# Optimization experiments

Measured on AMD Instinct MI355X. Metric: run time of the kernel, lower is better.

## Reference

```python
import jax, jax.numpy as jnp
import numpy as np

B, Cin, Cout, H, W, K = 8, 256, 256, 64, 64, 3  # kernel 3x3, stride 1, pad 1, dilation 1
EPS = 1e-5


def setup_inputs() -> dict:
    key = jax.random.key(0)
    k0, k1, k2 = jax.random.split(key, 3)
    x = jax.random.normal(k0, (B, Cin, H, W), jnp.float32)
    # offset-predicting conv (mmcv zero-inits it; use small random weights so offsets are nontrivial)
    w_off = jax.random.normal(k1, (2 * K * K, Cin, K, K), jnp.float32) * 0.01
    b_off = jnp.zeros((2 * K * K,), jnp.float32)
    # main deformable conv weight
    w = jax.random.normal(k2, (Cout, Cin, K, K), jnp.float32) * (1.0 / np.sqrt(Cin * K * K))
    b = jnp.zeros((Cout,), jnp.float32)
    gamma = jnp.ones((Cout,), jnp.float32)
    beta = jnp.zeros((Cout,), jnp.float32)
    return {"x": x, "w_off": w_off, "b_off": b_off, "w": w, "b": b, "gamma": gamma, "beta": beta}


def _deform_fusion(x, w_off, b_off, w, b, gamma, beta):
    Bn, C, Hh, Ww = x.shape
    # 1) predict offsets: [B, 2*K*K, H, W]; channel layout is (dy, dx) per kernel tap
    offset = jax.lax.conv_general_dilated(x, w_off, (1, 1), ((1, 1), (1, 1)))
    offset = offset + b_off[None, :, None, None]
    off = offset.reshape(Bn, K * K, 2, Hh, Ww)
    dy, dx = off[:, :, 0], off[:, :, 1]  # each [B, K*K, H, W]

    # 2) sampling positions: p = p0 + p_k + delta_p  (stride 1, pad 1 -> p_k in {-1,0,1})
    kk = jnp.arange(K * K)
    ky = (kk // K - (K // 2)).astype(jnp.float32)[None, :, None, None]
    kx = (kk % K - (K // 2)).astype(jnp.float32)[None, :, None, None]
    py = ky + jnp.arange(Hh, dtype=jnp.float32)[None, None, :, None] + dy  # [B,K2,H,W]
    px = kx + jnp.arange(Ww, dtype=jnp.float32)[None, None, None, :] + dx

    # 3) bilinear sampling with zero padding outside the image
    y0 = jnp.floor(py); x0 = jnp.floor(px)
    fy = py - y0; fx = px - x0
    x_flat = x.reshape(Bn, C, Hh * Ww)

    def corner(yi, xi, wgt):
        valid = (yi >= 0) & (yi <= Hh - 1) & (xi >= 0) & (xi <= Ww - 1)
        idx = (jnp.clip(yi, 0, Hh - 1) * Ww + jnp.clip(xi, 0, Ww - 1)).astype(jnp.int32)
        idx = idx.reshape(Bn, -1)  # [B, K2*H*W]
        g = jax.vmap(lambda xf, ii: jnp.take(xf, ii, axis=1))(x_flat, idx)  # [B,C,K2*H*W]
        return g * (wgt * valid).reshape(Bn, 1, -1)

    sampled = (corner(y0,     x0,     (1 - fy) * (1 - fx))
             + corner(y0,     x0 + 1, (1 - fy) * fx)
             + corner(y0 + 1, x0,     fy * (1 - fx))
             + corner(y0 + 1, x0 + 1, fy * fx))  # [B, C, K2*H*W]
    sampled = sampled.reshape(Bn, C, K * K, Hh * Ww)

    # 4) contract sampled patches with conv weight: implicit-GEMM of deformable conv
    out = jnp.einsum('bckp,ock->bop', sampled, w.reshape(w.shape[0], C, K * K))
    out = out + b[None, :, None]
    out = out.reshape(Bn, -1, Hh, Ww)

    # 5) BatchNorm (training-mode batch statistics) + ReLU
    mean = out.mean(axis=(0, 2, 3), keepdims=True)
    var = out.var(axis=(0, 2, 3), keepdims=True)
    out = gamma[None, :, None, None] * (out - mean) * jax.lax.rsqrt(var + EPS) + beta[None, :, None, None]
    return jax.nn.relu(out)


def reference(x, w_off, b_off, w, b, gamma, beta):
    return _deform_fusion(x, w_off, b_off, w, b, gamma, beta)
```

## Files before the change

### kernel.cpp

```cpp
#include <hip/hip_runtime.h>
#include <math.h>

#define BN_ 8
#define CIN 256
#define COUT 256
#define HH 64
#define WW 64
#define HW 4096
#define KK 9
#define OC 18
#define EPS 1e-5f
#define NTOT (BN_ * COUT * HW)

#define OFF_WS 0
#define WTB_WS 589824
#define WOB_WS 884736
#define ST_WS  921600
#define XT_WS  922112

typedef float f32x4 __attribute__((ext_vector_type(4)));
typedef short s16x8 __attribute__((ext_vector_type(8)));

__device__ __forceinline__ unsigned short f2bf(float f) {
  unsigned int u = __float_as_uint(f);
  unsigned int r = (u + 0x7fffu + ((u >> 16) & 1u)) >> 16;
  return (unsigned short)r;
}
__device__ __forceinline__ float bf2f(short s) {
  return __uint_as_float(((unsigned int)(unsigned short)s) << 16);
}

__global__ __launch_bounds__(256) void xpose_kernel(
    const float* __restrict__ x, unsigned short* __restrict__ xt) {
  __shared__ float s[64][65];
  const int t = threadIdx.x;
  const int p0 = blockIdx.x * 64;
  const int c0 = blockIdx.y * 64;
  const int b  = blockIdx.z;
  const float* xb = x + ((size_t)b * CIN + c0) * HW + p0;
#pragma unroll
  for (int pass = 0; pass < 4; ++pass) {
    int cr = pass * 16 + (t >> 4);
    int ps = (t & 15) * 4;
    float4 v = *(const float4*)(xb + (size_t)cr * HW + ps);
    s[ps + 0][cr] = v.x; s[ps + 1][cr] = v.y; s[ps + 2][cr] = v.z; s[ps + 3][cr] = v.w;
  }
  __syncthreads();
  unsigned short* xo = xt + (size_t)b * 32 * HW * 8;
#pragma unroll
  for (int r = 0; r < 2; ++r) {
    int flat = r * 256 + t;
    int pr = flat >> 3, sub = flat & 7;
    int g8 = (c0 >> 3) + sub;
    s16x8 v;
#pragma unroll
    for (int j = 0; j < 8; ++j) v[j] = (short)f2bf(s[pr][sub * 8 + j]);
    *(s16x8*)(xo + ((size_t)g8 * HW + p0 + pr) * 8) = v;
  }
}

__global__ __launch_bounds__(256) void wob_kernel(
    const float* __restrict__ w_off, unsigned short* __restrict__ wob) {
  const int ki = blockIdx.x;
  const int kk = ki >> 3;
  const int cc0 = (ki & 7) << 5;
#pragma unroll
  for (int r = 0; r < 4; ++r) {
    int e = r * 256 + threadIdx.x;
    int g = e >> 8, m = (e >> 3) & 31, j = e & 7;
    int c = cc0 + g * 8 + j;
    unsigned short v = 0;
    if (m < OC) v = f2bf(w_off[((size_t)m * CIN + c) * 9 + kk]);
    wob[(size_t)ki * 1024 + e] = v;
  }
}

__global__ __launch_bounds__(256) void offset_kernel(
    const unsigned short* __restrict__ xt, const unsigned short* __restrict__ wob,
    const float* __restrict__ b_off, float* __restrict__ off_ws) {
  __shared__ __align__(16) char smem[32768];
  const int t = threadIdx.x;
  const int lane = t & 63;
  const int wv = t >> 6;
  const int b = blockIdx.x & 7;
  const int h = blockIdx.x >> 3;
  const unsigned short* xtb = xt + (size_t)b * 32 * HW * 8;
  const int fr = lane & 15, fq = lane >> 4;
  unsigned short* sb = (unsigned short*)smem + wv * 2048;
  float* red = (float*)smem;

  f32x4 acc[2][4] = {};

  for (int s = 0; s < 18; ++s) {
    const int ki = wv * 18 + s;
    const int kk = ki >> 3, cc0 = (ki & 7) << 5;
    const int ky = kk / 3 - 1, kx = kk % 3 - 1;
    const int y = h + ky;
    const bool yok = (y >= 0) && (y < HH);
    const int xcol = lane + kx;
    const bool ok = yok && (xcol >= 0) && (xcol < WW);
    const int pix = y * WW + xcol;

    s16x8 af[2];
    const unsigned short* ap = wob + (size_t)ki * 1024;
#pragma unroll
    for (int i = 0; i < 2; ++i)
      af[i] = *(const s16x8*)&ap[(fq * 32 + i * 16 + fr) * 8];

#pragma unroll
    for (int g = 0; g < 4; ++g) {
      s16x8 v = {0, 0, 0, 0, 0, 0, 0, 0};
      if (ok)
        __builtin_memcpy(&v, (const char*)xtb + ((((size_t)(cc0 >> 3) + g) << 16)) + (size_t)pix * 16, 16);
      *(s16x8*)&sb[(g * 64 + lane) * 8] = v;
    }
    __builtin_amdgcn_s_waitcnt(0);

    s16x8 bf[4];
#pragma unroll
    for (int jn = 0; jn < 4; ++jn)
      bf[jn] = *(const s16x8*)&sb[(fq * 64 + jn * 16 + fr) * 8];
#pragma unroll
    for (int i = 0; i < 2; ++i)
#pragma unroll
      for (int jn = 0; jn < 4; ++jn)
        acc[i][jn] = __builtin_amdgcn_mfma_f32_16x16x32_bf16(af[i], bf[jn], acc[i][jn], 0, 0, 0);
  }

  __syncthreads();
#pragma unroll
  for (int i = 0; i < 2; ++i)
#pragma unroll
    for (int jn = 0; jn < 4; ++jn)
#pragma unroll
      for (int rg = 0; rg < 4; ++rg)
        red[wv * 2048 + (i * 16 + fq * 4 + rg) * 64 + jn * 16 + fr] = acc[i][jn][rg];
  __syncthreads();

  const int m = t >> 3;
  const int pq = (t & 7) * 8;
  float4 v0 = make_float4(0.f, 0.f, 0.f, 0.f), v1 = v0;
#pragma unroll
  for (int w = 0; w < 4; ++w) {
    float4 a = *(float4*)&red[w * 2048 + m * 64 + pq];
    float4 c = *(float4*)&red[w * 2048 + m * 64 + pq + 4];
    v0.x += a.x; v0.y += a.y; v0.z += a.z; v0.w += a.w;
    v1.x += c.x; v1.y += c.y; v1.z += c.z; v1.w += c.w;
  }
  if (m < OC) {
    float bo = b_off[m];
    v0.x += bo; v0.y += bo; v0.z += bo; v0.w += bo;
    v1.x += bo; v1.y += bo; v1.z += bo; v1.w += bo;
    float* op = off_ws + ((size_t)b * OC + m) * HW + h * WW + pq;
    *(float4*)op = v0;
    *(float4*)(op + 4) = v1;
  }
}

__global__ __launch_bounds__(256) void wtrans_kernel(
    const float* __restrict__ w, unsigned short* __restrict__ wTb) {
  const int kb = blockIdx.x;
  const int kk = kb >> 3;
  const int c0 = (kb & 7) << 5;
  const int o = threadIdx.x;
#pragma unroll
  for (int g = 0; g < 4; ++g)
#pragma unroll
    for (int j = 0; j < 8; ++j) {
      int c = c0 + g * 8 + j;
      wTb[(((size_t)kb * 4 + g) * 256 + o) * 8 + j] =
          f2bf(w[((size_t)o * CIN + c) * 9 + kk]);
    }
}

__global__ __launch_bounds__(256) void gemm_kernel(
    const unsigned short* __restrict__ xt, const unsigned short* __restrict__ wTb,
    const float* __restrict__ off_ws, const float* __restrict__ bias,
    float* __restrict__ out, float* __restrict__ stats) {
  __shared__ unsigned short s_b[2][2048];
  const int t = threadIdx.x;
  const int lane = t & 63;
  const int wv = t >> 6;
  const int b = blockIdx.x & 7;
  const int h = blockIdx.x >> 3;
  const int p0 = h * 64;
  const int col = t & 63;
  const int oct = t >> 6;
  const int fr = lane & 15, fq = lane >> 4;
  const unsigned short* xtb = xt + (size_t)b * 32 * HW * 8;
  const float* offp = off_ws + (size_t)b * OC * HW + p0 + col;

  int cofs[4];
  float qw[4], qwN[4];

  auto calc = [&](int kk, float dy, float dx) {
    float py = (float)(kk / 3 - 1 + h) + dy;
    float pxx = (float)(kk % 3 - 1 + col) + dx;
    float y0f = floorf(py), x0f = floorf(pxx);
    float fy = py - y0f, fx = pxx - x0f;
    int y0 = (int)y0f, x0 = (int)x0f;
    int y1 = y0 + 1, x1 = x0 + 1;
    bool vy0 = (y0 >= 0) && (y0 < HH), vy1 = (y1 >= 0) && (y1 < HH);
    bool vx0 = (x0 >= 0) && (x0 < WW), vx1 = (x1 >= 0) && (x1 < WW);
    int cy0 = min(max(y0, 0), HH - 1), cy1 = min(max(y1, 0), HH - 1);
    int cx0 = min(max(x0, 0), WW - 1), cx1 = min(max(x1, 0), WW - 1);
    cofs[0] = (cy0 * WW + cx0) * 16;  qwN[0] = (vy0 && vx0) ? (1.f - fy) * (1.f - fx) : 0.f;
    cofs[1] = (cy0 * WW + cx1) * 16;  qwN[1] = (vy0 && vx1) ? (1.f - fy) * fx : 0.f;
    cofs[2] = (cy1 * WW + cx0) * 16;  qwN[2] = (vy1 && vx0) ? fy * (1.f - fx) : 0.f;
    cofs[3] = (cy1 * WW + cx1) * 16;  qwN[3] = (vy1 && vx1) ? fy * fx : 0.f;
  };

  s16x8 gE[4], gO[4];
  s16x8 afE[4], afO[4];

  auto gather = [&](int c0c, s16x8* g) {
    const char* bp = (const char*)xtb + (((size_t)(c0c >> 3) + oct) << 16);
#pragma unroll
    for (int k = 0; k < 4; ++k)
      __builtin_memcpy(&g[k], bp + cofs[k], 16);
  };

  auto combine_write = [&](int buf, const s16x8* g) {
    s16x8 v;
#pragma unroll
    for (int j = 0; j < 8; ++j) {
      float val = 0.f;
#pragma unroll
      for (int k = 0; k < 4; ++k)
        val = fmaf(qw[k], bf2f(g[k][j]), val);
      v[j] = (short)f2bf(val);
    }
    *(s16x8*)&s_b[buf][(oct * 64 + col) * 8] = v;
  };

  auto load_a = [&](int iter, s16x8* af) {
    const unsigned short* ap = wTb + (((size_t)iter * 4 + fq) * 256 + wv * 64 + fr) * 8;
#pragma unroll
    for (int i = 0; i < 4; ++i)
      af[i] = *(const s16x8*)(ap + (size_t)i * 16 * 8);
  };

  f32x4 acc[4][4] = {};
  float dyp, dxp;

  {
    float dy0 = offp[0];
    float dx0 = offp[HW];
    calc(0, dy0, dx0);
#pragma unroll
    for (int k2 = 0; k2 < 4; ++k2) qw[k2] = qwN[k2];
    dyp = offp[2 * HW];
    dxp = offp[3 * HW];
    load_a(0, afE);
    gather(0, gE);
    gather(32, gO);
    combine_write(0, gE);
  }
  asm volatile("s_waitcnt lgkmcnt(0)" ::: "memory");
  __builtin_amdgcn_s_barrier();

#define GBODY(I, AFR, AFL, GW, GR, CUR)                                        \
  {                                                                            \
    s16x8 bfr[4];                                                              \
    _Pragma("unroll")                                                          \
    for (int j = 0; j < 4; ++j)                                                \
      bfr[j] = *(const s16x8*)&s_b[CUR][(fq * 64 + j * 16 + fr) * 8];          \
    const int nx1 = (I) + 1, nx2 = (I) + 2;                                    \
    bool newq = false;                                                         \
    if (nx1 < 72) {                                                            \
      load_a(nx1, AFL);                                                        \
      if (nx2 < 72) {                                                          \
        if ((nx2 & 7) == 0) {                                                  \
          const int kkc = nx2 >> 3;                                            \
          calc(kkc, dyp, dxp);                                                 \
          newq = true;                                                         \
          const int kkn = kkc + 1;                                             \
          if (kkn < 9) {                                                       \
            dyp = offp[(size_t)(2 * kkn) * HW];                                \
            dxp = offp[(size_t)(2 * kkn + 1) * HW];                            \
          }                                                                    \
        }                                                                      \
        gather((nx2 & 7) << 5, GW);                                            \
      }                                                                        \
    }                                                                          \
    _Pragma("unroll")                                                          \
    for (int ii = 0; ii < 4; ++ii)                                             \
      _Pragma("unroll")                                                        \
      for (int jj = 0; jj < 4; ++jj)                                           \
        acc[ii][jj] = __builtin_amdgcn_mfma_f32_16x16x32_bf16(                 \
            AFR[ii], bfr[jj], acc[ii][jj], 0, 0, 0);                           \
    if (nx1 < 72) {                                                            \
      combine_write((CUR) ^ 1, GR);                                            \
      if (newq) {                                                              \
        _Pragma("unroll")                                                      \
        for (int k2 = 0; k2 < 4; ++k2) qw[k2] = qwN[k2];                       \
      }                                                                        \
    }                                                                          \
    asm volatile("s_waitcnt lgkmcnt(0)" ::: "memory");                         \
    __builtin_amdgcn_s_barrier();                                              \
  }

  for (int m = 0; m < 36; ++m) {
    const int i0 = 2 * m;
    GBODY(i0, afE, afO, gE, gO, 0)
    GBODY(i0 + 1, afO, afE, gO, gE, 1)
  }
#undef GBODY

#pragma unroll
  for (int i = 0; i < 4; ++i) {
#pragma unroll
    for (int rg = 0; rg < 4; ++rg) {
      int o = wv * 64 + i * 16 + fq * 4 + rg;
      float bv = bias[o];
      float* op = out + ((size_t)(b * COUT + o)) * HW + p0 + fr;
      float s = 0.f, s2 = 0.f;
#pragma unroll
      for (int j = 0; j < 4; ++j) {
        float val = acc[i][j][rg] + bv;
        op[j * 16] = val;
        s += val; s2 += val * val;
      }
#pragma unroll
      for (int m2 = 1; m2 < 16; m2 <<= 1) {
        s += __shfl_xor(s, m2);
        s2 += __shfl_xor(s2, m2);
      }
      if (fr == 0) {
        atomicAdd(&stats[o], s);
        atomicAdd(&stats[COUT + o], s2);
      }
    }
  }
}

__global__ __launch_bounds__(256) void bn_kernel(
    float* __restrict__ out, const float* __restrict__ stats,
    const float* __restrict__ gamma, const float* __restrict__ beta) {
  int i4 = (blockIdx.x * 256 + threadIdx.x) * 4;
  int o = (i4 >> 12) & (COUT - 1);
  const float inv_n = 1.f / (float)(BN_ * HW);
  float mean = stats[o] * inv_n;
  float var = stats[COUT + o] * inv_n - mean * mean;
  float sc = gamma[o] * rsqrtf(var + EPS);
  float sh = beta[o] - mean * sc;
  float4 v = *(float4*)(out + i4);
  v.x = fmaxf(fmaf(v.x, sc, sh), 0.f);
  v.y = fmaxf(fmaf(v.y, sc, sh), 0.f);
  v.z = fmaxf(fmaf(v.z, sc, sh), 0.f);
  v.w = fmaxf(fmaf(v.w, sc, sh), 0.f);
  *(float4*)(out + i4) = v;
}

extern "C" void kernel_launch(void* const* d_in, const int* in_sizes, int n_in,
                              void* d_out, int out_size, void* d_ws, size_t ws_size,
                              hipStream_t stream) {
  const float* x     = (const float*)d_in[0];
  const float* w_off = (const float*)d_in[1];
  const float* b_off = (const float*)d_in[2];
  const float* w     = (const float*)d_in[3];
  const float* bias  = (const float*)d_in[4];
  const float* gamma = (const float*)d_in[5];
  const float* beta  = (const float*)d_in[6];
  float* out = (float*)d_out;
  float* ws = (float*)d_ws;
  float* off_ws = ws + OFF_WS;
  unsigned short* wTb = (unsigned short*)(ws + WTB_WS);
  unsigned short* wob = (unsigned short*)(ws + WOB_WS);
  float* stats = ws + ST_WS;
  unsigned short* xt = (unsigned short*)(ws + XT_WS);

  hipMemsetAsync(stats, 0, 2 * COUT * sizeof(float), stream);
  xpose_kernel<<<dim3(64, 4, 8), 256, 0, stream>>>(x, xt);
  wob_kernel<<<72, 256, 0, stream>>>(w_off, wob);
  wtrans_kernel<<<72, 256, 0, stream>>>(w, wTb);
  offset_kernel<<<512, 256, 0, stream>>>(xt, wob, b_off, off_ws);
  gemm_kernel<<<512, 256, 0, stream>>>(xt, wTb, off_ws, bias, out, stats);
  bn_kernel<<<NTOT / 1024, 256, 0, stream>>>(out, stats, gamma, beta);
}
```

Baseline: 234.6 us.

## Double gemm block to 512 threads, halving per-wave output tile and K iterations

The deformable GEMM block now runs 8 waves instead of 4. Each wave owns 32 output channels instead of 64, and each iteration covers 64 input channels instead of 32, so there are 36 iterations rather than 72. Eight threads per column gather the bilinear samples, which spreads gather and combine work over more threads. The weight fragments are no longer prefetched one iteration ahead; they are loaded at the start of each iteration. B fragments are read from LDS inside the MFMA loop. The goal is more latency hiding and fewer barriers, at the cost of weight loads that are no longer prefetched and more LDS per block.

```diff
diff --git a/kernel.cpp b/kernel.cpp
--- a/kernel.cpp
+++ b/kernel.cpp
@@ -173,11 +173,11 @@
     }
 }
 
-__global__ __launch_bounds__(256) void gemm_kernel(
+__global__ __launch_bounds__(512, 4) void gemm_kernel(
     const unsigned short* __restrict__ xt, const unsigned short* __restrict__ wTb,
     const float* __restrict__ off_ws, const float* __restrict__ bias,
     float* __restrict__ out, float* __restrict__ stats) {
-  __shared__ unsigned short s_b[2][2048];
+  __shared__ unsigned short s_b[2][4096];
   const int t = threadIdx.x;
   const int lane = t & 63;
   const int wv = t >> 6;
@@ -211,10 +211,9 @@
   };
 
   s16x8 gE[4], gO[4];
-  s16x8 afE[4], afO[4];
-
-  auto gather = [&](int c0c, s16x8* g) {
-    const char* bp = (const char*)xtb + (((size_t)(c0c >> 3) + oct) << 16);
+
+  auto gather = [&](int chunk64, s16x8* g) {
+    const char* bp = (const char*)xtb + (((size_t)(chunk64 * 8 + oct)) << 16);
 #pragma unroll
     for (int k = 0; k < 4; ++k)
       __builtin_memcpy(&g[k], bp + cofs[k], 16);
@@ -233,14 +232,18 @@
     *(s16x8*)&s_b[buf][(oct * 64 + col) * 8] = v;
   };
 
-  auto load_a = [&](int iter, s16x8* af) {
-    const unsigned short* ap = wTb + (((size_t)iter * 4 + fq) * 256 + wv * 64 + fr) * 8;
-#pragma unroll
-    for (int i = 0; i < 4; ++i)
-      af[i] = *(const s16x8*)(ap + (size_t)i * 16 * 8);
+  auto load_a = [&](int iter, s16x8 af[2][2]) {
+#pragma unroll
+    for (int ks = 0; ks < 2; ++ks) {
+      const unsigned short* ap =
+          wTb + (((size_t)(iter * 2 + ks) * 4 + fq) * 256 + wv * 32 + fr) * 8;
+#pragma unroll
+      for (int i = 0; i < 2; ++i)
+        af[ks][i] = *(const s16x8*)(ap + (size_t)i * 16 * 8);
+    }
   };
 
-  f32x4 acc[4][4] = {};
+  f32x4 acc[2][4] = {};
   float dyp, dxp;
 
   {
@@ -251,27 +254,23 @@
     for (int k2 = 0; k2 < 4; ++k2) qw[k2] = qwN[k2];
     dyp = offp[2 * HW];
     dxp = offp[3 * HW];
-    load_a(0, afE);
     gather(0, gE);
-    gather(32, gO);
+    gather(1, gO);
     combine_write(0, gE);
   }
   asm volatile("s_waitcnt lgkmcnt(0)" ::: "memory");
   __builtin_amdgcn_s_barrier();
 
-#define GBODY(I, AFR, AFL, GW, GR, CUR)                                        \
+#define GBODY(I, GW, GR, CUR)                                                  \
   {                                                                            \
-    s16x8 bfr[4];                                                              \
-    _Pragma("unroll")                                                          \
-    for (int j = 0; j < 4; ++j)                                                \
-      bfr[j] = *(const s16x8*)&s_b[CUR][(fq * 64 + j * 16 + fr) * 8];          \
+    s16x8 af[2][2];                                                            \
+    load_a(I, af);                                                             \
     const int nx1 = (I) + 1, nx2 = (I) + 2;                                    \
     bool newq = false;                                                         \
-    if (nx1 < 72) {                                                            \
-      load_a(nx1, AFL);                                                        \
-      if (nx2 < 72) {                                                          \
-        if ((nx2 & 7) == 0) {                                                  \
-          const int kkc = nx2 >> 3;                                            \
+    if (nx1 < 36) {                                                            \
+      if (nx2 < 36) {                                                          \
+        if ((nx2 & 3) == 0) {                                                  \
+          const int kkc = nx2 >> 2;                                            \
           calc(kkc, dyp, dxp);                                                 \
           newq = true;                                                         \
           const int kkn = kkc + 1;                                             \
@@ -280,38 +279,40 @@
             dxp = offp[(size_t)(2 * kkn + 1) * HW];                            \
           }                                                                    \
         }                                                                      \
-        gather((nx2 & 7) << 5, GW);                                            \
+        gather((nx2) & 3, GW);                                                 \
       }                                                                        \
-    }                                                                          \
-    _Pragma("unroll")                                                          \
-    for (int ii = 0; ii < 4; ++ii)                                             \
-      _Pragma("unroll")                                                        \
-      for (int jj = 0; jj < 4; ++jj)                                           \
-        acc[ii][jj] = __builtin_amdgcn_mfma_f32_16x16x32_bf16(                 \
-            AFR[ii], bfr[jj], acc[ii][jj], 0, 0, 0);                           \
-    if (nx1 < 72) {                                                            \
       combine_write((CUR) ^ 1, GR);                                            \
       if (newq) {                                                              \
         _Pragma("unroll")                                                      \
         for (int k2 = 0; k2 < 4; ++k2) qw[k2] = qwN[k2];                       \
       }                                                                        \
     }                                                                          \
+    _Pragma("unroll")                                                          \
+    for (int ks = 0; ks < 2; ++ks)                                             \
+      _Pragma("unroll")                                                        \
+      for (int jj = 0; jj < 4; ++jj) {                                         \
+        s16x8 bfr = *(const s16x8*)&s_b[CUR][((ks * 4 + fq) * 64 + jj * 16 + fr) * 8]; \
+        _Pragma("unroll")                                                      \
+        for (int ii = 0; ii < 2; ++ii)                                         \
+          acc[ii][jj] = __builtin_amdgcn_mfma_f32_16x16x32_bf16(               \
+              af[ks][ii], bfr, acc[ii][jj], 0, 0, 0);                          \
+      }                                                                        \
     asm volatile("s_waitcnt lgkmcnt(0)" ::: "memory");                         \
     __builtin_amdgcn_s_barrier();                                              \
   }
 
-  for (int m = 0; m < 36; ++m) {
+  for (int m = 0; m < 18; ++m) {
     const int i0 = 2 * m;
-    GBODY(i0, afE, afO, gE, gO, 0)
-    GBODY(i0 + 1, afO, afE, gO, gE, 1)
+    GBODY(i0, gE, gO, 0)
+    GBODY(i0 + 1, gO, gE, 1)
   }
 #undef GBODY
 
 #pragma unroll
-  for (int i = 0; i < 4; ++i) {
+  for (int i = 0; i < 2; ++i) {
 #pragma unroll
     for (int rg = 0; rg < 4; ++rg) {
-      int o = wv * 64 + i * 16 + fq * 4 + rg;
+      int o = wv * 32 + i * 16 + fq * 4 + rg;
       float bv = bias[o];
       float* op = out + ((size_t)(b * COUT + o)) * HW + p0 + fr;
       float s = 0.f, s2 = 0.f;
@@ -375,6 +376,6 @@
   wob_kernel<<<72, 256, 0, stream>>>(w_off, wob);
   wtrans_kernel<<<72, 256, 0, stream>>>(w, wTb);
   offset_kernel<<<512, 256, 0, stream>>>(xt, wob, b_off, off_ws);
-  gemm_kernel<<<512, 256, 0, stream>>>(xt, wTb, off_ws, bias, out, stats);
+  gemm_kernel<<<512, 512, 0, stream>>>(xt, wTb, off_ws, bias, out, stats);
   bn_kernel<<<NTOT / 1024, 256, 0, stream>>>(out, stats, gamma, beta);
 }
```

After: 229.8 us. 2.1% less time.
